# Optimization experiments

Hardware: AMD Instinct MI355X
Metric: run time of the kernel (lower is better)

## Reference

```python
import jax, jax.numpy as jnp
import numpy as np

N = 172032          # total anchor points (8 images x 21504)
C = 256             # prompt classes
REG_MAX = 16        # DFL bins
M = 64              # GT boxes
IMG = 1024.0
RADIUS = 0.75       # center_sampling_radius
SIGMA = 2.0         # heat sigma
ALPHA, GAMMA = 0.75, 2.0  # varifocal
MARGIN = 8.0
AREA_THR = 0.6
EPS = 1e-6


def setup_inputs() -> dict:
    key = jax.random.key(0)
    ks = jax.random.split(key, 10)
    anchor_points = jax.random.uniform(ks[0], (N, 2)) * IMG
    cls_logits = jax.random.normal(ks[1], (N, C))
    target_scores = jax.random.uniform(ks[2], (N, C))
    pred_dist = jax.random.normal(ks[3], (N, 4, REG_MAX))
    dfl_target = jax.random.uniform(ks[4], (N, 4)) * (REG_MAX - 1)
    # valid xyxy GT boxes inside the image
    xy = jax.random.uniform(ks[5], (M, 2)) * (IMG - 200.0)
    wh = jax.random.uniform(ks[6], (M, 2)) * 180.0 + 20.0
    gt_boxes = jnp.concatenate([xy, xy + wh], axis=-1)
    box_weights = jax.random.uniform(ks[7], (M,))
    pred_boxes = jax.random.uniform(ks[8], (N, 4)) * IMG
    obj_logits = jax.random.normal(ks[9], (N,))
    return {"anchor_points": anchor_points, "cls_logits": cls_logits,
            "target_scores": target_scores, "pred_dist": pred_dist,
            "dfl_target": dfl_target, "gt_boxes": gt_boxes,
            "box_weights": box_weights, "pred_boxes": pred_boxes,
            "obj_logits": obj_logits}


def _inside_and_delta(ap, boxes):
    # ap [N,2], boxes [M,4] -> inside [M,N], delta [M,N,2], half_size [M,1,2]
    inside = ((ap[None, :, 0] >= boxes[:, None, 0]) & (ap[None, :, 0] <= boxes[:, None, 2]) &
              (ap[None, :, 1] >= boxes[:, None, 1]) & (ap[None, :, 1] <= boxes[:, None, 3]))
    center = (boxes[:, :2] + boxes[:, 2:]) * 0.5          # [M,2]
    half = jnp.clip((boxes[:, 2:] - boxes[:, :2]) * 0.5, 1.0)
    delta = (ap[None, :, :] - center[:, None, :]) / half[:, None, :]  # [M,N,2]
    return inside, delta


def build_box_region_weights(ap, boxes, bw, radius):
    inside, delta = _inside_and_delta(ap, boxes)
    center_mask = jnp.max(jnp.abs(delta), axis=-1) <= radius           # [M,N]
    cand = inside & center_mask
    has_cand = jnp.any(cand, axis=1, keepdims=True)
    cand = jnp.where(has_cand, cand, inside)                           # fallback to inside
    return jnp.max(cand.astype(bw.dtype) * bw[:, None], axis=0)        # [N]


def build_center_heat_targets(ap, boxes, sigma):
    sigma = max(float(sigma), 0.001)
    inside, delta = _inside_and_delta(ap, boxes)
    heat = jnp.exp(-0.5 * jnp.sum((delta / sigma) ** 2, axis=-1))      # [M,N]
    heat = heat * inside.astype(heat.dtype)
    return jnp.clip(jnp.max(heat, axis=0), 0.0, 1.0)                   # [N]


def sigmoid_varifocal_loss(logits, targets, alpha, gamma):
    prob = jax.nn.sigmoid(logits)
    weight = alpha * prob ** gamma * (1.0 - targets) + targets
    # stable BCE-with-logits
    bce = jnp.maximum(logits, 0.0) - logits * targets + jnp.log1p(jnp.exp(-jnp.abs(logits)))
    return bce * weight


def dfl_loss(pred_dist, target, reg_max):
    # pred_dist [N,4,R], target [N,4] float in [0, R-1]
    tl = jnp.clip(target.astype(jnp.int32), 0, reg_max - 1)
    tr = jnp.clip(tl + 1, 0, reg_max - 1)
    wl = tr.astype(target.dtype) - target
    wr = 1.0 - wl
    logp = jax.nn.log_softmax(pred_dist, axis=-1)
    ll = -jnp.take_along_axis(logp, tl[..., None], axis=-1)[..., 0]
    lr = -jnp.take_along_axis(logp, tr[..., None], axis=-1)[..., 0]
    return ll * wl + lr * wr                                           # [N,4]


def weighted_mean(loss, weights):
    while weights.ndim < loss.ndim:
        weights = weights[..., None]
    return jnp.sum(loss * weights) / jnp.clip(jnp.sum(weights), EPS)


def oversize_box_penalty(boxes, image_size, area_threshold):
    x1 = jnp.clip(boxes[:, 0], 0.0, image_size)
    y1 = jnp.clip(boxes[:, 1], 0.0, image_size)
    x2 = jnp.clip(boxes[:, 2], 0.0, image_size)
    y2 = jnp.clip(boxes[:, 3], 0.0, image_size)
    w = jnp.clip(x2 - x1, 0.0)
    h = jnp.clip(y2 - y1, 0.0)
    area_ratio = w * h / max(float(image_size * image_size), 1.0)
    edge = ((x1 <= 1.0).astype(boxes.dtype) + (y1 <= 1.0).astype(boxes.dtype) +
            (x2 >= image_size - 1.0).astype(boxes.dtype) + (y2 >= image_size - 1.0).astype(boxes.dtype)) / 4.0
    return jnp.clip(area_ratio - area_threshold, 0.0) * (1.0 + edge)


def reference(anchor_points, cls_logits, target_scores, pred_dist, dfl_target,
              gt_boxes, box_weights, pred_boxes, obj_logits):
    region_w = build_box_region_weights(anchor_points, gt_boxes, box_weights, RADIUS)  # [N]
    heat = build_center_heat_targets(anchor_points, gt_boxes, SIGMA)                   # [N]

    vfl = sigmoid_varifocal_loss(cls_logits, target_scores, ALPHA, GAMMA)              # [N,C]
    cls_loss = weighted_mean(vfl, region_w + heat)

    obj_bce = jnp.maximum(obj_logits, 0.0) - obj_logits * heat + jnp.log1p(jnp.exp(-jnp.abs(obj_logits)))
    obj_loss = jnp.mean(obj_bce)

    dfl = dfl_loss(pred_dist, dfl_target, REG_MAX)                                     # [N,4]
    box_dfl_loss = weighted_mean(dfl, region_w)

    penalty = jnp.mean(oversize_box_penalty(pred_boxes, IMG, AREA_THR))
    margin = jnp.mean(jax.nn.relu(jnp.max(cls_logits, axis=-1) - MARGIN))

    total = cls_loss + obj_loss + box_dfl_loss + 0.1 * penalty + 0.05 * margin
    return total
```

## Files before the change

### kernel.cpp

```cpp
#include <hip/hip_runtime.h>

#define MM 64
#define MAIN_BLOCKS 1344
#define PREP_BLOCKS 672
#define NQ_MAIN 5
#define NQ_PREP 2

__device__ __forceinline__ float vfl1(float l, float t, float* vmax) {
    float e = __expf(-l);
    float p = __fdividef(1.0f, 1.0f + e);
    float q = fmaxf(p, 1.0f - p);
    float bce = fmaf(-l, t, fmaxf(l, 0.0f)) - __logf(q);
    float wgt = fmaf(0.75f * p * p, 1.0f - t, t);
    *vmax = fmaxf(*vmax, l);
    return bce * wgt;
}

__global__ __launch_bounds__(256) void k_hascand(
    const float2* __restrict__ ap, const float4* __restrict__ boxes,
    unsigned long long* __restrict__ mask, int n_pts)
{
    __shared__ float4 sb[MM];
    if (threadIdx.x < MM) sb[threadIdx.x] = boxes[threadIdx.x];
    __syncthreads();
    unsigned long long local = 0ull;
    int stride = gridDim.x * blockDim.x;
    for (int n = blockIdx.x * blockDim.x + threadIdx.x; n < n_pts; n += stride) {
        float2 p = ap[n];
        for (int m = 0; m < MM; ++m) {
            float4 b = sb[m];
            if (p.x >= b.x && p.x <= b.z && p.y >= b.y && p.y <= b.w) {
                float hx = fmaxf((b.z - b.x) * 0.5f, 1.0f);
                float hy = fmaxf((b.w - b.y) * 0.5f, 1.0f);
                float dx = fabsf(p.x - (b.x + b.z) * 0.5f) / hx;
                float dy = fabsf(p.y - (b.y + b.w) * 0.5f) / hy;
                if (fmaxf(dx, dy) <= 0.75f) local |= (1ull << m);
            }
        }
    }
    #pragma unroll
    for (int o = 32; o; o >>= 1) local |= __shfl_xor(local, o);
    if ((threadIdx.x & 63) == 0 && local) atomicOr(mask, local);
}

__global__ __launch_bounds__(256) void k_prep(
    const float2* __restrict__ ap, const float4* __restrict__ boxes,
    const float* __restrict__ bw, const unsigned long long* __restrict__ candmask,
    const float4* __restrict__ pboxes, const float* __restrict__ obj,
    float2* __restrict__ w2, float* __restrict__ prep_partials, int n_pts)
{
    __shared__ float4 sB[MM];
    __shared__ float4 sA[MM];
    __shared__ float  sW[MM];
    if (threadIdx.x < MM) {
        float4 b = boxes[threadIdx.x];
        sB[threadIdx.x] = b;
        float ihx = __fdividef(1.0f, fmaxf((b.z - b.x) * 0.5f, 1.0f));
        float ihy = __fdividef(1.0f, fmaxf((b.w - b.y) * 0.5f, 1.0f));
        sA[threadIdx.x] = make_float4((b.x + b.z) * 0.5f, (b.y + b.w) * 0.5f, ihx, ihy);
        sW[threadIdx.x] = bw[threadIdx.x];
    }
    __syncthreads();
    unsigned long long cm = candmask[0];
    int n = blockIdx.x * blockDim.x + threadIdx.x;
    float aObj = 0.f, aPen = 0.f;
    if (n < n_pts) {
        float2 p = ap[n];
        float rw = 0.f, ht = 0.f;
        #pragma unroll 8
        for (int m = 0; m < MM; ++m) {
            float4 b = sB[m];
            float4 a = sA[m];
            bool inside = (p.x >= b.x) & (p.x <= b.z) & (p.y >= b.y) & (p.y <= b.w);
            float dx = (p.x - a.x) * a.z;
            float dy = (p.y - a.y) * a.w;
            bool cand = inside && (fmaxf(fabsf(dx), fabsf(dy)) <= 0.75f);
            bool eff = ((cm >> m) & 1ull) ? cand : inside;
            if (eff) rw = fmaxf(rw, sW[m]);
            float h = __expf(-0.125f * (dx * dx + dy * dy));
            if (inside) ht = fmaxf(ht, h);
        }
        ht = fminf(ht, 1.0f);
        w2[n] = make_float2(rw + ht, rw);

        float ol = obj[n];
        aObj = fmaxf(ol, 0.f) - ol * ht + __logf(1.0f + __expf(-fabsf(ol)));

        float4 pbx = pboxes[n];
        float x1 = fminf(fmaxf(pbx.x, 0.f), 1024.0f);
        float y1 = fminf(fmaxf(pbx.y, 0.f), 1024.0f);
        float x2 = fminf(fmaxf(pbx.z, 0.f), 1024.0f);
        float y2 = fminf(fmaxf(pbx.w, 0.f), 1024.0f);
        float wq = fmaxf(x2 - x1, 0.f), hq = fmaxf(y2 - y1, 0.f);
        float ar = wq * hq * (1.0f / (1024.0f * 1024.0f));
        float edge = ((x1 <= 1.f ? 1.f : 0.f) + (y1 <= 1.f ? 1.f : 0.f) +
                      (x2 >= 1023.f ? 1.f : 0.f) + (y2 >= 1023.f ? 1.f : 0.f)) * 0.25f;
        aPen = fmaxf(ar - 0.6f, 0.f) * (1.f + edge);
    }
    #pragma unroll
    for (int o = 32; o; o >>= 1) {
        aObj += __shfl_xor(aObj, o);
        aPen += __shfl_xor(aPen, o);
    }
    __shared__ float sh[4][2];
    int lane = threadIdx.x & 63, wid = threadIdx.x >> 6;
    if (lane == 0) { sh[wid][0] = aObj; sh[wid][1] = aPen; }
    __syncthreads();
    if (threadIdx.x < NQ_PREP) {
        prep_partials[blockIdx.x * NQ_PREP + threadIdx.x] =
            sh[0][threadIdx.x] + sh[1][threadIdx.x] + sh[2][threadIdx.x] + sh[3][threadIdx.x];
    }
}

__global__ __launch_bounds__(256) void k_main(
    const float4* __restrict__ cls4,
    const float4* __restrict__ ts4,
    const float4* __restrict__ pd4,
    const float*  __restrict__ dflt,
    const float2* __restrict__ w2,
    float* __restrict__ partials,
    int n_pts)
{
    const int tid  = threadIdx.x;
    const int lane = tid & 63;
    const int wid  = tid >> 6;
    const int wave = blockIdx.x * 4 + wid;
    const int base = wave * 32;

    const int a_off = lane >> 4;
    const int r_idx = (lane & 15) >> 2;
    const float j0  = (float)(4 * (lane & 3));

    float accS1 = 0.f, accS2 = 0.f, accS3 = 0.f, accS4 = 0.f, accMar = 0.f;

    #pragma unroll 1
    for (int blk = 0; blk < 4; ++blk) {
        const int n0 = base + blk * 8;
        float4 c4[8], s4[8];
        #pragma unroll
        for (int c = 0; c < 8; ++c) {
            int idx = (n0 + c) * 64 + lane;
            c4[c] = cls4[idx];
            s4[c] = ts4[idx];
        }
        float4 p4[2];
        #pragma unroll
        for (int c = 0; c < 2; ++c) p4[c] = pd4[n0 * 16 + c * 64 + lane];
        float2 wv = w2[n0 + (lane & 7)];
        float tgv[2];
        #pragma unroll
        for (int c = 0; c < 2; ++c)
            tgv[c] = dflt[(n0 + c * 4 + a_off) * 4 + r_idx];

        #pragma unroll
        for (int c = 0; c < 8; ++c) {
            float w  = __shfl(wv.x, c);
            float rw = __shfl(wv.y, c);
            float vmax = -1e30f;
            float vs = vfl1(c4[c].x, s4[c].x, &vmax) + vfl1(c4[c].y, s4[c].y, &vmax)
                     + vfl1(c4[c].z, s4[c].z, &vmax) + vfl1(c4[c].w, s4[c].w, &vmax);
            accS1 = fmaf(w, vs, accS1);
            accS2 += w;
            accS4 += rw;
            if (__any(vmax > 8.0f)) {
                float t = vmax;
                #pragma unroll
                for (int o = 32; o; o >>= 1) t = fmaxf(t, __shfl_xor(t, o));
                accMar += t - 8.0f;
            }
        }

        #pragma unroll
        for (int c = 0; c < 2; ++c) {
            float4 x = p4[c];
            float se = __expf(x.x) + __expf(x.y) + __expf(x.z) + __expf(x.w);
            se += __shfl_xor(se, 1);
            se += __shfl_xor(se, 2);
            float lse = __logf(se);
            float tg = tgv[c];
            float tx = 0.f;
            tx = fmaf(fmaxf(1.0f - fabsf(tg - j0), 0.f),          x.x, tx);
            tx = fmaf(fmaxf(1.0f - fabsf(tg - (j0 + 1.f)), 0.f),  x.y, tx);
            tx = fmaf(fmaxf(1.0f - fabsf(tg - (j0 + 2.f)), 0.f),  x.z, tx);
            tx = fmaf(fmaxf(1.0f - fabsf(tg - (j0 + 3.f)), 0.f),  x.w, tx);
            float rwl = __shfl(wv.y, c * 4 + a_off);
            accS3 = fmaf(rwl, 0.25f * lse - tx, accS3);
        }
    }

    #pragma unroll
    for (int o = 32; o; o >>= 1) {
        accS1 += __shfl_xor(accS1, o);
        accS3 += __shfl_xor(accS3, o);
    }
    __shared__ float sh[4][NQ_MAIN];
    if (lane == 0) {
        sh[wid][0] = accS1; sh[wid][1] = accS2; sh[wid][2] = accS3;
        sh[wid][3] = accS4; sh[wid][4] = accMar;
    }
    __syncthreads();
    if (tid < NQ_MAIN) {
        partials[blockIdx.x * NQ_MAIN + tid] =
            sh[0][tid] + sh[1][tid] + sh[2][tid] + sh[3][tid];
    }
}

__global__ __launch_bounds__(256) void k_final(
    const float* __restrict__ mainp, const float* __restrict__ prepp,
    float* __restrict__ out, int n_pts)
{
    double acc[7];
    #pragma unroll
    for (int q = 0; q < 7; ++q) acc[q] = 0.0;
    for (int i = threadIdx.x; i < MAIN_BLOCKS; i += 256) {
        #pragma unroll
        for (int q = 0; q < NQ_MAIN; ++q) acc[q] += (double)mainp[i * NQ_MAIN + q];
    }
    for (int i = threadIdx.x; i < PREP_BLOCKS; i += 256) {
        #pragma unroll
        for (int q = 0; q < NQ_PREP; ++q) acc[5 + q] += (double)prepp[i * NQ_PREP + q];
    }
    __shared__ double sh[256][8];
    #pragma unroll
    for (int q = 0; q < 7; ++q) sh[threadIdx.x][q] = acc[q];
    __syncthreads();
    for (int s = 128; s; s >>= 1) {
        if (threadIdx.x < s) {
            #pragma unroll
            for (int q = 0; q < 7; ++q) sh[threadIdx.x][q] += sh[threadIdx.x + s][q];
        }
        __syncthreads();
    }
    if (threadIdx.x == 0) {
        double S1 = sh[0][0], S2 = sh[0][1], S3 = sh[0][2], S4 = sh[0][3];
        double Sm = sh[0][4], So = sh[0][5], Sp = sh[0][6];
        double invN = 1.0 / (double)n_pts;
        double cls_loss = S1 / fmax(S2, 1e-6);
        double dfl_loss = S3 / fmax(S4, 1e-6);
        out[0] = (float)(cls_loss + So * invN + dfl_loss + 0.1 * Sp * invN + 0.05 * Sm * invN);
    }
}

extern "C" void kernel_launch(void* const* d_in, const int* in_sizes, int n_in,
                              void* d_out, int out_size, void* d_ws, size_t ws_size,
                              hipStream_t stream) {
    const float2* ap    = (const float2*)d_in[0];
    const float4* cls4  = (const float4*)d_in[1];
    const float4* ts4   = (const float4*)d_in[2];
    const float4* pd4   = (const float4*)d_in[3];
    const float*  dflt  = (const float*)d_in[4];
    const float4* boxes = (const float4*)d_in[5];
    const float*  bw    = (const float*)d_in[6];
    const float4* pbx   = (const float4*)d_in[7];
    const float*  obj   = (const float*)d_in[8];
    int n_pts = in_sizes[0] / 2;

    unsigned long long* mask = (unsigned long long*)d_ws;
    float* main_partials = (float*)((char*)d_ws + 1024);
    float* prep_partials = (float*)((char*)d_ws + 32768);
    float2* w2 = (float2*)((char*)d_ws + 65536);

    hipMemsetAsync(d_ws, 0, 16, stream);
    k_hascand<<<256, 256, 0, stream>>>(ap, boxes, mask, n_pts);
    k_prep<<<PREP_BLOCKS, 256, 0, stream>>>(ap, boxes, bw, mask, pbx, obj, w2,
                                            prep_partials, n_pts);
    k_main<<<MAIN_BLOCKS, 256, 0, stream>>>(cls4, ts4, pd4, dflt, w2,
                                            main_partials, n_pts);
    k_final<<<1, 256, 0, stream>>>(main_partials, prep_partials, (float*)d_out, n_pts);
}
```

Measured before the change: 142.8 us.

## Fuse region-weight prep kernel into main loss kernel, splitting box loop across half-waves

Removes the separate k_prep kernel. Each wave now computes the region weight and heat for its own 32 anchors inside k_main, with the two half-waves each scanning 32 of the 64 boxes and merging through a shuffle. The objectness and penalty sums are folded into the main partials, so the w2 workspace round-trip and one kernel launch go away. In exchange, the box-loop ALU work now runs before the main streaming loads, which may delay memory issue in each wave.

```diff
diff --git a/kernel.cpp b/kernel.cpp
--- a/kernel.cpp
+++ b/kernel.cpp
@@ -2,9 +2,7 @@
 
 #define MM 64
 #define MAIN_BLOCKS 1344
-#define PREP_BLOCKS 672
-#define NQ_MAIN 5
-#define NQ_PREP 2
+#define NQ 7
 
 __device__ __forceinline__ float vfl1(float l, float t, float* vmax) {
     float e = __expf(-l);
@@ -43,11 +41,19 @@
     if ((threadIdx.x & 63) == 0 && local) atomicOr(mask, local);
 }
 
-__global__ __launch_bounds__(256) void k_prep(
-    const float2* __restrict__ ap, const float4* __restrict__ boxes,
-    const float* __restrict__ bw, const unsigned long long* __restrict__ candmask,
-    const float4* __restrict__ pboxes, const float* __restrict__ obj,
-    float2* __restrict__ w2, float* __restrict__ prep_partials, int n_pts)
+__global__ __launch_bounds__(256) void k_main(
+    const float2* __restrict__ ap,
+    const float4* __restrict__ cls4,
+    const float4* __restrict__ ts4,
+    const float4* __restrict__ pd4,
+    const float*  __restrict__ dflt,
+    const float4* __restrict__ boxes,
+    const float*  __restrict__ bw,
+    const float4* __restrict__ pboxes,
+    const float*  __restrict__ obj,
+    const unsigned long long* __restrict__ candmask,
+    float* __restrict__ partials,
+    int n_pts)
 {
     __shared__ float4 sB[MM];
     __shared__ float4 sA[MM];
@@ -60,33 +66,44 @@
         sA[threadIdx.x] = make_float4((b.x + b.z) * 0.5f, (b.y + b.w) * 0.5f, ihx, ihy);
         sW[threadIdx.x] = bw[threadIdx.x];
     }
-    __syncthreads();
-    unsigned long long cm = candmask[0];
-    int n = blockIdx.x * blockDim.x + threadIdx.x;
+
+    const int tid  = threadIdx.x;
+    const int lane = tid & 63;
+    const int wid  = tid >> 6;
+    const int wave = blockIdx.x * 4 + wid;
+    const int base = wave * 32;
+    const unsigned long long cm = candmask[0];
+    __syncthreads();
+
+    const int la = lane & 31;
+    const int na = base + la;
+    const int mbase = (lane >> 5) << 5;
+    float2 p = ap[na];
+    float rw = 0.f, ht = 0.f;
+    #pragma unroll 8
+    for (int mm = 0; mm < 32; ++mm) {
+        int m = mbase + mm;
+        float4 b = sB[m];
+        float4 a = sA[m];
+        bool inside = (p.x >= b.x) & (p.x <= b.z) & (p.y >= b.y) & (p.y <= b.w);
+        float dx = (p.x - a.x) * a.z;
+        float dy = (p.y - a.y) * a.w;
+        bool cand = inside && (fmaxf(fabsf(dx), fabsf(dy)) <= 0.75f);
+        bool eff = ((cm >> m) & 1ull) ? cand : inside;
+        if (eff) rw = fmaxf(rw, sW[m]);
+        float h = __expf(-0.125f * (dx * dx + dy * dy));
+        if (inside) ht = fmaxf(ht, h);
+    }
+    rw = fmaxf(rw, __shfl_xor(rw, 32));
+    ht = fminf(fmaxf(ht, __shfl_xor(ht, 32)), 1.0f);
+    const float wvx = rw + ht;
+    const float wvy = rw;
+
     float aObj = 0.f, aPen = 0.f;
-    if (n < n_pts) {
-        float2 p = ap[n];
-        float rw = 0.f, ht = 0.f;
-        #pragma unroll 8
-        for (int m = 0; m < MM; ++m) {
-            float4 b = sB[m];
-            float4 a = sA[m];
-            bool inside = (p.x >= b.x) & (p.x <= b.z) & (p.y >= b.y) & (p.y <= b.w);
-            float dx = (p.x - a.x) * a.z;
-            float dy = (p.y - a.y) * a.w;
-            bool cand = inside && (fmaxf(fabsf(dx), fabsf(dy)) <= 0.75f);
-            bool eff = ((cm >> m) & 1ull) ? cand : inside;
-            if (eff) rw = fmaxf(rw, sW[m]);
-            float h = __expf(-0.125f * (dx * dx + dy * dy));
-            if (inside) ht = fmaxf(ht, h);
-        }
-        ht = fminf(ht, 1.0f);
-        w2[n] = make_float2(rw + ht, rw);
-
-        float ol = obj[n];
+    if (lane < 32) {
+        float ol = obj[na];
         aObj = fmaxf(ol, 0.f) - ol * ht + __logf(1.0f + __expf(-fabsf(ol)));
-
-        float4 pbx = pboxes[n];
+        float4 pbx = pboxes[na];
         float x1 = fminf(fmaxf(pbx.x, 0.f), 1024.0f);
         float y1 = fminf(fmaxf(pbx.y, 0.f), 1024.0f);
         float x2 = fminf(fmaxf(pbx.z, 0.f), 1024.0f);
@@ -97,35 +114,6 @@
                       (x2 >= 1023.f ? 1.f : 0.f) + (y2 >= 1023.f ? 1.f : 0.f)) * 0.25f;
         aPen = fmaxf(ar - 0.6f, 0.f) * (1.f + edge);
     }
-    #pragma unroll
-    for (int o = 32; o; o >>= 1) {
-        aObj += __shfl_xor(aObj, o);
-        aPen += __shfl_xor(aPen, o);
-    }
-    __shared__ float sh[4][2];
-    int lane = threadIdx.x & 63, wid = threadIdx.x >> 6;
-    if (lane == 0) { sh[wid][0] = aObj; sh[wid][1] = aPen; }
-    __syncthreads();
-    if (threadIdx.x < NQ_PREP) {
-        prep_partials[blockIdx.x * NQ_PREP + threadIdx.x] =
-            sh[0][threadIdx.x] + sh[1][threadIdx.x] + sh[2][threadIdx.x] + sh[3][threadIdx.x];
-    }
-}
-
-__global__ __launch_bounds__(256) void k_main(
-    const float4* __restrict__ cls4,
-    const float4* __restrict__ ts4,
-    const float4* __restrict__ pd4,
-    const float*  __restrict__ dflt,
-    const float2* __restrict__ w2,
-    float* __restrict__ partials,
-    int n_pts)
-{
-    const int tid  = threadIdx.x;
-    const int lane = tid & 63;
-    const int wid  = tid >> 6;
-    const int wave = blockIdx.x * 4 + wid;
-    const int base = wave * 32;
 
     const int a_off = lane >> 4;
     const int r_idx = (lane & 15) >> 2;
@@ -146,7 +134,6 @@
         float4 p4[2];
         #pragma unroll
         for (int c = 0; c < 2; ++c) p4[c] = pd4[n0 * 16 + c * 64 + lane];
-        float2 wv = w2[n0 + (lane & 7)];
         float tgv[2];
         #pragma unroll
         for (int c = 0; c < 2; ++c)
@@ -154,14 +141,14 @@
 
         #pragma unroll
         for (int c = 0; c < 8; ++c) {
-            float w  = __shfl(wv.x, c);
-            float rw = __shfl(wv.y, c);
+            float w   = __shfl(wvx, blk * 8 + c);
+            float rw_ = __shfl(wvy, blk * 8 + c);
             float vmax = -1e30f;
             float vs = vfl1(c4[c].x, s4[c].x, &vmax) + vfl1(c4[c].y, s4[c].y, &vmax)
                      + vfl1(c4[c].z, s4[c].z, &vmax) + vfl1(c4[c].w, s4[c].w, &vmax);
             accS1 = fmaf(w, vs, accS1);
             accS2 += w;
-            accS4 += rw;
+            accS4 += rw_;
             if (__any(vmax > 8.0f)) {
                 float t = vmax;
                 #pragma unroll
@@ -183,7 +170,7 @@
             tx = fmaf(fmaxf(1.0f - fabsf(tg - (j0 + 1.f)), 0.f),  x.y, tx);
             tx = fmaf(fmaxf(1.0f - fabsf(tg - (j0 + 2.f)), 0.f),  x.z, tx);
             tx = fmaf(fmaxf(1.0f - fabsf(tg - (j0 + 3.f)), 0.f),  x.w, tx);
-            float rwl = __shfl(wv.y, c * 4 + a_off);
+            float rwl = __shfl(wvy, blk * 8 + c * 4 + a_off);
             accS3 = fmaf(rwl, 0.25f * lse - tx, accS3);
         }
     }
@@ -192,42 +179,40 @@
     for (int o = 32; o; o >>= 1) {
         accS1 += __shfl_xor(accS1, o);
         accS3 += __shfl_xor(accS3, o);
-    }
-    __shared__ float sh[4][NQ_MAIN];
+        aObj  += __shfl_xor(aObj, o);
+        aPen  += __shfl_xor(aPen, o);
+    }
+    __shared__ float sh[4][NQ];
     if (lane == 0) {
         sh[wid][0] = accS1; sh[wid][1] = accS2; sh[wid][2] = accS3;
-        sh[wid][3] = accS4; sh[wid][4] = accMar;
-    }
-    __syncthreads();
-    if (tid < NQ_MAIN) {
-        partials[blockIdx.x * NQ_MAIN + tid] =
+        sh[wid][3] = accS4; sh[wid][4] = accMar; sh[wid][5] = aObj;
+        sh[wid][6] = aPen;
+    }
+    __syncthreads();
+    if (tid < NQ) {
+        partials[blockIdx.x * NQ + tid] =
             sh[0][tid] + sh[1][tid] + sh[2][tid] + sh[3][tid];
     }
 }
 
 __global__ __launch_bounds__(256) void k_final(
-    const float* __restrict__ mainp, const float* __restrict__ prepp,
-    float* __restrict__ out, int n_pts)
+    const float* __restrict__ mainp, float* __restrict__ out, int n_pts)
 {
-    double acc[7];
-    #pragma unroll
-    for (int q = 0; q < 7; ++q) acc[q] = 0.0;
+    double acc[NQ];
+    #pragma unroll
+    for (int q = 0; q < NQ; ++q) acc[q] = 0.0;
     for (int i = threadIdx.x; i < MAIN_BLOCKS; i += 256) {
         #pragma unroll
-        for (int q = 0; q < NQ_MAIN; ++q) acc[q] += (double)mainp[i * NQ_MAIN + q];
-    }
-    for (int i = threadIdx.x; i < PREP_BLOCKS; i += 256) {
-        #pragma unroll
-        for (int q = 0; q < NQ_PREP; ++q) acc[5 + q] += (double)prepp[i * NQ_PREP + q];
-    }
-    __shared__ double sh[256][8];
-    #pragma unroll
-    for (int q = 0; q < 7; ++q) sh[threadIdx.x][q] = acc[q];
+        for (int q = 0; q < NQ; ++q) acc[q] += (double)mainp[i * NQ + q];
+    }
+    __shared__ double sh[256][NQ + 1];
+    #pragma unroll
+    for (int q = 0; q < NQ; ++q) sh[threadIdx.x][q] = acc[q];
     __syncthreads();
     for (int s = 128; s; s >>= 1) {
         if (threadIdx.x < s) {
             #pragma unroll
-            for (int q = 0; q < 7; ++q) sh[threadIdx.x][q] += sh[threadIdx.x + s][q];
+            for (int q = 0; q < NQ; ++q) sh[threadIdx.x][q] += sh[threadIdx.x + s][q];
         }
         __syncthreads();
     }
@@ -257,14 +242,10 @@
 
     unsigned long long* mask = (unsigned long long*)d_ws;
     float* main_partials = (float*)((char*)d_ws + 1024);
-    float* prep_partials = (float*)((char*)d_ws + 32768);
-    float2* w2 = (float2*)((char*)d_ws + 65536);
 
     hipMemsetAsync(d_ws, 0, 16, stream);
     k_hascand<<<256, 256, 0, stream>>>(ap, boxes, mask, n_pts);
-    k_prep<<<PREP_BLOCKS, 256, 0, stream>>>(ap, boxes, bw, mask, pbx, obj, w2,
-                                            prep_partials, n_pts);
-    k_main<<<MAIN_BLOCKS, 256, 0, stream>>>(cls4, ts4, pd4, dflt, w2,
-                                            main_partials, n_pts);
-    k_final<<<1, 256, 0, stream>>>(main_partials, prep_partials, (float*)d_out, n_pts);
-}
+    k_main<<<MAIN_BLOCKS, 256, 0, stream>>>(ap, cls4, ts4, pd4, dflt, boxes, bw,
+                                            pbx, obj, mask, main_partials, n_pts);
+    k_final<<<1, 256, 0, stream>>>(main_partials, (float*)d_out, n_pts);
+}
```

Result: faster. 136.6 us (-4.3%).
